# Optimization experiments

Hardware: AMD Instinct MI355X
Metric: run time of the kernel (lower is better)

Reference implementation:

```python
import jax, jax.numpy as jnp
import numpy as np

B, T, C_IN, DIM, NFFT, HOP = 8, 1024, 256, 512, 1024, 256
NOUT = NFFT // 2 + 1
BB_DIL = (1, 1, 2, 2, 4, 4, 8, 8)
RES_DIL = (1, 3, 5)
N_RES = 3


def conv1d(x, w, b, dilation=1, groups=1, padding=0):
    # x: (B,C,T), w: (O, I/groups, K)
    y = jax.lax.conv_general_dilated(
        x, w, window_strides=(1,), padding=[(padding, padding)],
        rhs_dilation=(dilation,), dimension_numbers=('NCH', 'OIH', 'NCH'),
        feature_group_count=groups)
    return y + b[None, :, None]


def layernorm(x, g, b, eps=1e-6):
    m = jnp.mean(x, -1, keepdims=True)
    v = jnp.mean((x - m) ** 2, -1, keepdims=True)
    return (x - m) * jax.lax.rsqrt(v + eps) * g + b


def istft(spec, window):
    # spec: (B, F, Tf) complex, center=True, hann window, win_length=n_fft
    Bsz, F_, Tf = spec.shape
    frames = jnp.fft.irfft(spec, n=NFFT, axis=1)            # (B, n_fft, Tf)
    frames = jnp.transpose(frames, (0, 2, 1)) * window       # (B, Tf, n_fft)
    L = NFFT + HOP * (Tf - 1)
    idx = jnp.arange(Tf)[:, None] * HOP + jnp.arange(NFFT)[None, :]  # (Tf, n_fft)
    y = jnp.zeros((Bsz, L), frames.dtype).at[:, idx].add(frames)
    env = jnp.zeros((L,), window.dtype).at[idx].add(
        jnp.broadcast_to(window ** 2, (Tf, NFFT)))
    y = y / jnp.where(env > 1e-11, env, 1.0)
    start = NFFT // 2
    return y[:, start:start + HOP * (Tf - 1)]


def setup_inputs() -> dict:
    key = jax.random.key(0)
    ks = iter(jax.random.split(key, 64))
    r = lambda *s: jax.random.normal(next(ks), s, jnp.float32) * 0.02
    return {
        'x': jax.random.normal(next(ks), (B, T, C_IN), jnp.float32),
        'conv_in_w': r(DIM, C_IN, 7), 'conv_in_b': r(DIM),
        'skip_w': r(DIM, C_IN, 1), 'skip_b': r(DIM),
        'bb_dw_w': r(8, DIM, 1, 7), 'bb_dw_b': r(8, DIM),
        'bb_ln_g': jnp.ones((8, DIM), jnp.float32), 'bb_ln_b': jnp.zeros((8, DIM), jnp.float32),
        'bb_pw1_w': r(8, 4 * DIM, DIM), 'bb_pw1_b': r(8, 4 * DIM),
        'bb_pw2_w': r(8, DIM, 4 * DIM), 'bb_pw2_b': r(8, DIM),
        'bb_gamma': jnp.full((8, DIM), 1e-6, jnp.float32),
        'res_w1': r(N_RES, 3, DIM, DIM, 3), 'res_b1': r(N_RES, 3, DIM),
        'res_w2': r(N_RES, 3, DIM, DIM, 3), 'res_b2': r(N_RES, 3, DIM),
        'ln_g': jnp.ones((DIM,), jnp.float32), 'ln_b': jnp.zeros((DIM,), jnp.float32),
        'mag_w1': r(DIM, DIM), 'mag_b1': r(DIM),
        'mag_w2': r(NOUT, DIM), 'mag_b2': r(NOUT),
        'ph_w': r(NOUT, DIM), 'ph_b': r(NOUT),
        'cumsum_w': jnp.linspace(0.05, 0.4, NOUT, dtype=jnp.float32)[None, :],
        'window': (0.5 - 0.5 * jnp.cos(2.0 * jnp.pi * jnp.arange(NFFT) / NFFT)).astype(jnp.float32),
    }


def reference(x, conv_in_w, conv_in_b, skip_w, skip_b,
              bb_dw_w, bb_dw_b, bb_ln_g, bb_ln_b,
              bb_pw1_w, bb_pw1_b, bb_pw2_w, bb_pw2_b, bb_gamma,
              res_w1, res_b1, res_w2, res_b2,
              ln_g, ln_b, mag_w1, mag_b1, mag_w2, mag_b2,
              ph_w, ph_b, cumsum_w, window):
    # (B,T,C) -> (B,C,T)
    h = jnp.transpose(x, (0, 2, 1))
    skip = conv1d(h, skip_w, skip_b)                     # (B,DIM,T)
    hp = jnp.pad(h, ((0, 0), (0, 0), (3, 3)), mode='reflect')
    h = conv1d(hp, conv_in_w, conv_in_b)                 # kernel 7, pad 0 -> (B,DIM,T)
    # ConvNeXt backbone
    for i, d in enumerate(BB_DIL):
        res = h
        pad = (7 + (d - 1) * 6) // 2
        y = conv1d(h, bb_dw_w[i], bb_dw_b[i], dilation=d, groups=DIM, padding=pad)
        y = jnp.transpose(y, (0, 2, 1))                  # (B,T,DIM)
        y = layernorm(y, bb_ln_g[i], bb_ln_b[i])
        y = jax.nn.gelu(y @ bb_pw1_w[i].T + bb_pw1_b[i], approximate=False)
        y = y @ bb_pw2_w[i].T + bb_pw2_b[i]
        y = bb_gamma[i] * y
        h = res + jnp.transpose(y, (0, 2, 1))
    h = h + skip                                         # same length T
    # Residual dilated conv stacks
    for i in range(N_RES):
        for j, d in enumerate(RES_DIL):
            y = conv1d(h, res_w1[i, j], res_b1[i, j], dilation=d, padding=d)
            y = jax.nn.leaky_relu(y, 0.1)
            y = conv1d(y, res_w2[i, j], res_b2[i, j], padding=1)
            h = h + y
    h = jnp.transpose(h, (0, 2, 1))                      # (B,T,DIM)
    h = layernorm(h, ln_g, ln_b)
    # magnitude head
    m = jax.nn.gelu(h @ mag_w1.T + mag_b1, approximate=False)
    log_mag = m @ mag_w2.T + mag_b2
    mag = jnp.exp(jnp.clip(log_mag, -10.0, 10.0))        # (B,T,NOUT)
    # instantaneous-frequency phase head
    inst = jnp.tanh(h @ ph_w.T + ph_b) * jnp.pi
    phase = jnp.cumsum(inst * cumsum_w, axis=1)
    phase = jnp.remainder(phase + jnp.pi, 2.0 * jnp.pi) - jnp.pi
    # synthesize
    spec = jax.lax.complex(mag * jnp.cos(phase), mag * jnp.sin(phase))
    spec = jnp.transpose(spec, (0, 2, 1))                # (B,F,T)
    return istft(spec, window)
```

## Files before the change

kernel.cpp:

```cpp
#include <hip/hip_runtime.h>
#include <math.h>

constexpr int Bv = 8, Tv = 1024, DIMC = 512, NOUTC = 513;
constexpr int Mrows = Bv * 1024;
constexpr int LDS_S = 1056;
constexpr float PI_F = 3.14159265358979323846f;
constexpr float TWOPI_F = 6.28318530717958647692f;

struct TapInfo { int n; int off[7]; };
struct PtrTable { _Float16* h[36]; };

enum { BND_NONE = 0, BND_ZERO, BND_REFLECT };

typedef _Float16 half8v __attribute__((ext_vector_type(8)));
typedef _Float16 half4v __attribute__((ext_vector_type(4)));
typedef float f32x4 __attribute__((ext_vector_type(4)));

__device__ __forceinline__ void gld_lds16(const void* g, void* l) {
  __builtin_amdgcn_global_load_lds(
      (const __attribute__((address_space(1))) unsigned int*)g,
      (__attribute__((address_space(3))) unsigned int*)l, 16, 0, 0);
}

__device__ __forceinline__ void xcd_tile(int TMpix, int TNpix, int& m0, int& n0) {
  const int lin = blockIdx.y * gridDim.x + blockIdx.x;
  const int cpx = (gridDim.x * gridDim.y) >> 3;
  const int nid = (lin & 7) * cpx + (lin >> 3);
  m0 = (nid / gridDim.y) * TMpix;
  n0 = (nid % gridDim.y) * TNpix;
}

enum { MEPI_GELU_H = 0, MEPI_GAMMARES };

template<int EPI, int TN>
__global__ __launch_bounds__(256)
void mfma_gemm(const _Float16* __restrict__ A, int lda,
               const _Float16* __restrict__ W, int K,
               const float* __restrict__ bias,
               const float* __restrict__ aux,
               float* __restrict__ hio,
               _Float16* __restrict__ Ch,
               int N, int ldc)
{
  constexpr int NFR = TN / 32;
  __shared__ _Float16 sA[2][128 * 32];
  __shared__ _Float16 sB[2][TN * 32];
  int m0, n0;
  xcd_tile(128, TN, m0, n0);
  const int tid = threadIdx.x;
  const int wid = tid >> 6, lane = tid & 63;
  const int wr = wid >> 1, wc = wid & 1;
  const int fr = lane & 15, fq = lane >> 4;

  f32x4 acc[4][NFR] = {};

  const int rbase = tid >> 2;
  const int kwS = (((tid & 3) ^ ((tid >> 3) & 3)) << 3);
  const int nkc = K >> 5;
  const int fqS = fq ^ ((fr >> 1) & 3);
  const int aBase = (wr * 64 + fr) * 32 + fqS * 8;
  const int bBase = (wc * (TN / 2) + fr) * 32 + fqS * 8;

  const _Float16* arow[2];
  #pragma unroll
  for (int s = 0; s < 2; ++s)
    arow[s] = A + (size_t)(m0 + s * 64 + rbase) * lda + kwS;

  auto STAGE = [&](int kc, int buf) {
    const int k0 = kc << 5;
    #pragma unroll
    for (int s = 0; s < 2; ++s)
      gld_lds16(arow[s] + k0, (char*)&sA[buf][0] + s * 4096 + wid * 1024);
    #pragma unroll
    for (int s = 0; s < TN / 64; ++s) {
      size_t bo = (size_t)(n0 + s * 64 + rbase) * K + kwS + k0;
      gld_lds16(W + bo, (char*)&sB[buf][0] + s * 4096 + wid * 1024);
    }
  };
  auto COMPUTE = [&](int buf) {
    half8v aF[4], bF[NFR];
    #pragma unroll
    for (int i = 0; i < 4; ++i) aF[i] = *(const half8v*)&sA[buf][aBase + i * 512];
    #pragma unroll
    for (int j = 0; j < NFR; ++j) bF[j] = *(const half8v*)&sB[buf][bBase + j * 512];
    #pragma unroll
    for (int i = 0; i < 4; ++i)
      #pragma unroll
      for (int j = 0; j < NFR; ++j)
        acc[i][j] = __builtin_amdgcn_mfma_f32_16x16x32_f16(aF[i], bF[j], acc[i][j], 0, 0, 0);
  };

  STAGE(0, 0);
  __syncthreads();
  int cur = 0;
  for (int kc = 0; kc < nkc; ++kc) {
    if (kc + 1 < nkc) STAGE(kc + 1, cur ^ 1);
    COMPUTE(cur);
    __syncthreads();
    cur ^= 1;
  }

  #pragma unroll
  for (int j = 0; j < NFR; ++j) {
    const int n = n0 + wc * (TN / 2) + j * 16 + fr;
    const float bj = bias[n];
    const float gj = (EPI == MEPI_GAMMARES) ? aux[n] : 0.f;
    #pragma unroll
    for (int i = 0; i < 4; ++i) {
      const int mB = m0 + wr * 64 + i * 16 + fq * 4;
      #pragma unroll
      for (int r = 0; r < 4; ++r) {
        const int m = mB + r;
        float v = acc[i][j][r] + bj;
        if (EPI == MEPI_GELU_H) {
          v = 0.5f * v * (1.f + erff(v * 0.70710678118654752f));
          Ch[(size_t)m * ldc + n] = (_Float16)v;
        } else {
          hio[(size_t)m * ldc + n] += gj * v;
        }
      }
    }
  }
}

enum { SEPI_F32 = 0, SEPI_LEAKY_SPLIT, SEPI_ADDRES_SPLIT,
       SEPI_GELU_SPLIT, SEPI_EXPCLIP, SEPI_TANHCW };

template<int EPI, int BND, int TN>
__global__ __launch_bounds__(256)
void mfma_gemm_split(const _Float16* __restrict__ Ah, const _Float16* __restrict__ Al, int lda,
                     const _Float16* __restrict__ Wh, const _Float16* __restrict__ Wl, int K,
                     const float* __restrict__ bias,
                     const float* __restrict__ aux,
                     float* __restrict__ hio,
                     float* __restrict__ Cf,
                     _Float16* __restrict__ Chh, _Float16* __restrict__ Chl,
                     int N, int ldc,
                     const _Float16* __restrict__ zpage,
                     TapInfo taps)
{
  constexpr int NFR = TN / 32;
  __shared__ _Float16 sAh[2][128 * 32];
  __shared__ _Float16 sAl[2][128 * 32];
  __shared__ _Float16 sBh[2][TN * 32];
  __shared__ _Float16 sBl[2][TN * 32];
  int m0, n0;
  xcd_tile(128, TN, m0, n0);
  const int tid = threadIdx.x;
  const int wid = tid >> 6, lane = tid & 63;
  const int wr = wid >> 1, wc = wid & 1;
  const int fr = lane & 15, fq = lane >> 4;

  f32x4 acc[4][NFR] = {};

  const int t0 = m0 & (Tv - 1);
  const int rbase = tid >> 2;
  const int kwS = (((tid & 3) ^ ((tid >> 3) & 3)) << 3);
  const int nkc = K >> 5;
  const int NT = taps.n * nkc;
  const int fqS = fq ^ ((fr >> 1) & 3);
  const int aBase = (wr * 64 + fr) * 32 + fqS * 8;
  const int bBase = (wc * (TN / 2) + fr) * 32 + fqS * 8;

  auto STAGE = [&](int st, int buf) {
    int tap = (taps.n == 1) ? 0 : (st / nkc);
    int kc = st - tap * nkc;
    const int k0 = kc << 5;
    const int off = (BND == BND_NONE) ? 0 : taps.off[tap];
    const _Float16* Wth = Wh + (size_t)tap * N * K;
    const _Float16* Wtl = Wl + (size_t)tap * N * K;
    #pragma unroll
    for (int s = 0; s < 2; ++s) {
      int t = t0 + s * 64 + rbase + off;
      bool valid = true;
      if (BND == BND_REFLECT) t = (t < 0) ? -t : (t >= Tv ? 2 * Tv - 2 - t : t);
      else if (BND == BND_ZERO) valid = (t >= 0) && (t < Tv);
      size_t ro = (size_t)(m0 - t0 + t) * lda + kwS + k0;
      const void* sh = valid ? (const void*)(Ah + ro) : (const void*)zpage;
      const void* sl = valid ? (const void*)(Al + ro) : (const void*)zpage;
      gld_lds16(sh, (char*)&sAh[buf][0] + s * 4096 + wid * 1024);
      gld_lds16(sl, (char*)&sAl[buf][0] + s * 4096 + wid * 1024);
    }
    #pragma unroll
    for (int s = 0; s < TN / 64; ++s) {
      size_t bo = (size_t)(n0 + s * 64 + rbase) * K + kwS + k0;
      gld_lds16(Wth + bo, (char*)&sBh[buf][0] + s * 4096 + wid * 1024);
      gld_lds16(Wtl + bo, (char*)&sBl[buf][0] + s * 4096 + wid * 1024);
    }
  };

  auto COMPUTE = [&](int buf) {
    half8v ah[4], al[4], bh[NFR], bl[NFR];
    #pragma unroll
    for (int i = 0; i < 4; ++i) {
      ah[i] = *(const half8v*)&sAh[buf][aBase + i * 512];
      al[i] = *(const half8v*)&sAl[buf][aBase + i * 512];
    }
    #pragma unroll
    for (int j = 0; j < NFR; ++j) {
      bh[j] = *(const half8v*)&sBh[buf][bBase + j * 512];
      bl[j] = *(const half8v*)&sBl[buf][bBase + j * 512];
    }
    #pragma unroll
    for (int i = 0; i < 4; ++i)
      #pragma unroll
      for (int j = 0; j < NFR; ++j) {
        acc[i][j] = __builtin_amdgcn_mfma_f32_16x16x32_f16(ah[i], bh[j], acc[i][j], 0, 0, 0);
        acc[i][j] = __builtin_amdgcn_mfma_f32_16x16x32_f16(ah[i], bl[j], acc[i][j], 0, 0, 0);
        acc[i][j] = __builtin_amdgcn_mfma_f32_16x16x32_f16(al[i], bh[j], acc[i][j], 0, 0, 0);
      }
  };

  STAGE(0, 0);
  __syncthreads();
  int cur = 0;
  for (int st = 0; st < NT; ++st) {
    if (st + 1 < NT) STAGE(st + 1, cur ^ 1);
    COMPUTE(cur);
    __syncthreads();
    cur ^= 1;
  }

  #pragma unroll
  for (int j = 0; j < NFR; ++j) {
    const int n = n0 + wc * (TN / 2) + j * 16 + fr;
    const bool nok = (n < N);
    const float bj = (nok && bias) ? bias[n] : 0.f;
    const float ax = (EPI == SEPI_TANHCW && nok) ? aux[n] : 0.f;
    #pragma unroll
    for (int i = 0; i < 4; ++i) {
      const int mB = m0 + wr * 64 + i * 16 + fq * 4;
      #pragma unroll
      for (int r = 0; r < 4; ++r) {
        const int m = mB + r;
        float v = acc[i][j][r] + bj;
        if (!nok) continue;
        if (EPI == SEPI_F32) {
          Cf[(size_t)m * ldc + n] = v;
        } else if (EPI == SEPI_GELU_SPLIT) {
          v = 0.5f * v * (1.f + erff(v * 0.70710678118654752f));
          _Float16 hi = (_Float16)v;
          Chh[(size_t)m * ldc + n] = hi;
          Chl[(size_t)m * ldc + n] = (_Float16)(v - (float)hi);
        } else if (EPI == SEPI_EXPCLIP) {
          Cf[(size_t)m * ldc + n] = expf(fminf(fmaxf(v, -10.f), 10.f));
        } else if (EPI == SEPI_TANHCW) {
          Cf[(size_t)m * ldc + n] = tanhf(v) * PI_F * ax;
        }
      }
    }
  }
}

enum { REPI_LEAKY = 0, REPI_ADDRES };

template<int EPI>
__global__ __launch_bounds__(256)
void res_gemm(const _Float16* __restrict__ Ah, const _Float16* __restrict__ Al,
              const _Float16* __restrict__ Wh, const _Float16* __restrict__ Wl,
              const float* __restrict__ bias,
              float* __restrict__ hio,
              _Float16* __restrict__ Chh, _Float16* __restrict__ Chl,
              const _Float16* __restrict__ zpage,
              int d)
{
  __shared__ _Float16 sAh_[160 * 32];
  __shared__ _Float16 sAl_[160 * 32];
  __shared__ _Float16 sB_[3 * 2 * 64 * 32];
  int m0, n0;
  xcd_tile(128, 64, m0, n0);
  const int tid = threadIdx.x;
  const int wid = tid >> 6, lane = tid & 63;
  const int wr = wid >> 1, wc = wid & 1;
  const int fr = lane & 15, fq = lane >> 4;
  const int t0 = m0 & (Tv - 1);

  f32x4 acc[4][2] = {};
  const int offs[3] = {-d, 0, d};

  for (int kc = 0; kc < 16; ++kc) {
    const int k0h = kc << 5;
    #pragma unroll
    for (int it = 0; it < 5; ++it) {
      int cb = it * 4 + wid;
      int half = (cb >= 10) ? 1 : 0;
      int rb = (cb - half * 10) * 16;
      int row = rb + (lane >> 2);
      int slot_g = (lane & 3) ^ ((row >> 1) & 3);
      int t = t0 - 16 + row;
      bool valid = (t >= 0) && (t < Tv);
      const _Float16* srcb = half ? Al : Ah;
      const void* src = valid
          ? (const void*)(srcb + (size_t)(m0 - t0 + t) * DIMC + k0h + slot_g * 8)
          : (const void*)(zpage + slot_g * 8);
      void* dst = (char*)(half ? sAl_ : sAh_) + rb * 64;
      gld_lds16(src, dst);
    }
    #pragma unroll
    for (int it = 0; it < 6; ++it) {
      int cb = it * 4 + wid;
      int tap = cb >> 3;
      int r2 = cb & 7;
      int half = r2 >> 2;
      int rb = (r2 & 3) * 16;
      int row = rb + (lane >> 2);
      int slot_g = (lane & 3) ^ ((row >> 1) & 3);
      const _Float16* srcb = (half ? Wl : Wh) + (size_t)tap * 512 * 512
                           + (size_t)(n0 + row) * 512 + k0h + slot_g * 8;
      void* dst = (char*)sB_ + ((size_t)(tap * 2 + half) * 64 + rb) * 64;
      gld_lds16(srcb, dst);
    }
    __syncthreads();

    #pragma unroll
    for (int tap = 0; tap < 3; ++tap) {
      const int off = offs[tap];
      half8v ah[4], al[4], bh[2], bl[2];
      #pragma unroll
      for (int i = 0; i < 4; ++i) {
        int rA = wr * 64 + i * 16 + fr + off + 16;
        int ab = rA * 64 + ((fq ^ ((rA >> 1) & 3)) * 16);
        ah[i] = *(const half8v*)((const char*)sAh_ + ab);
        al[i] = *(const half8v*)((const char*)sAl_ + ab);
      }
      #pragma unroll
      for (int j = 0; j < 2; ++j) {
        int rB = wc * 32 + j * 16 + fr;
        int bb = rB * 64 + ((fq ^ ((rB >> 1) & 3)) * 16);
        bh[j] = *(const half8v*)((const char*)sB_ + (tap * 2 + 0) * 4096 + bb);
        bl[j] = *(const half8v*)((const char*)sB_ + (tap * 2 + 1) * 4096 + bb);
      }
      #pragma unroll
      for (int i = 0; i < 4; ++i)
        #pragma unroll
        for (int j = 0; j < 2; ++j) {
          acc[i][j] = __builtin_amdgcn_mfma_f32_16x16x32_f16(ah[i], bh[j], acc[i][j], 0, 0, 0);
          acc[i][j] = __builtin_amdgcn_mfma_f32_16x16x32_f16(ah[i], bl[j], acc[i][j], 0, 0, 0);
          acc[i][j] = __builtin_amdgcn_mfma_f32_16x16x32_f16(al[i], bh[j], acc[i][j], 0, 0, 0);
        }
    }
    __syncthreads();
  }

  #pragma unroll
  for (int j = 0; j < 2; ++j) {
    const int n = n0 + wc * 32 + j * 16 + fr;
    const float bj = bias[n];
    #pragma unroll
    for (int i = 0; i < 4; ++i) {
      const int mB = m0 + wr * 64 + i * 16 + fq * 4;
      #pragma unroll
      for (int r = 0; r < 4; ++r) {
        const int m = mB + r;
        float v = acc[i][j][r] + bj;
        if (EPI == REPI_LEAKY) {
          v = (v > 0.f) ? v : 0.1f * v;
          _Float16 hi = (_Float16)v;
          Chh[(size_t)m * DIMC + n] = hi;
          Chl[(size_t)m * DIMC + n] = (_Float16)(v - (float)hi);
        } else {
          float nh = hio[(size_t)m * DIMC + n] + v;
          hio[(size_t)m * DIMC + n] = nh;
          _Float16 hi = (_Float16)nh;
          Chh[(size_t)m * DIMC + n] = hi;
          Chl[(size_t)m * DIMC + n] = (_Float16)(nh - (float)hi);
        }
      }
    }
  }
}

__global__ __launch_bounds__(256)
void convin_gemm(const _Float16* __restrict__ Ah, const _Float16* __restrict__ Al,
                 const _Float16* __restrict__ Wh, const _Float16* __restrict__ Wl,
                 const float* __restrict__ bias,
                 float* __restrict__ Cf)
{
  __shared__ _Float16 sAh_[160 * 32];
  __shared__ _Float16 sAl_[160 * 32];
  __shared__ _Float16 sB_[7 * 2 * 64 * 32];
  int m0, n0;
  xcd_tile(128, 64, m0, n0);
  const int tid = threadIdx.x;
  const int wid = tid >> 6, lane = tid & 63;
  const int wr = wid >> 1, wc = wid & 1;
  const int fr = lane & 15, fq = lane >> 4;
  const int t0 = m0 & (Tv - 1);

  f32x4 acc[4][2] = {};

  for (int kc = 0; kc < 8; ++kc) {
    const int k0h = kc << 5;
    #pragma unroll
    for (int it = 0; it < 5; ++it) {
      int cb = it * 4 + wid;
      int half = (cb >= 10) ? 1 : 0;
      int rb = (cb - half * 10) * 16;
      int row = rb + (lane >> 2);
      int slot_g = (lane & 3) ^ ((row >> 1) & 3);
      int t = t0 - 16 + row;
      t = (t < 0) ? -t : (t >= Tv ? 2 * Tv - 2 - t : t);
      const _Float16* srcb = half ? Al : Ah;
      const void* src = srcb + (size_t)(m0 - t0 + t) * 256 + k0h + slot_g * 8;
      void* dst = (char*)(half ? sAl_ : sAh_) + rb * 64;
      gld_lds16(src, dst);
    }
    #pragma unroll
    for (int it = 0; it < 14; ++it) {
      int cb = it * 4 + wid;
      int tap = cb >> 3;
      int r2 = cb & 7;
      int half = r2 >> 2;
      int rb = (r2 & 3) * 16;
      int row = rb + (lane >> 2);
      int slot_g = (lane & 3) ^ ((row >> 1) & 3);
      const _Float16* srcb = (half ? Wl : Wh) + (size_t)tap * 512 * 256
                           + (size_t)(n0 + row) * 256 + k0h + slot_g * 8;
      void* dst = (char*)sB_ + ((size_t)(tap * 2 + half) * 64 + rb) * 64;
      gld_lds16(srcb, dst);
    }
    __syncthreads();

    #pragma unroll
    for (int tap = 0; tap < 7; ++tap) {
      const int off = tap - 3;
      half8v ah[4], al[4], bh[2], bl[2];
      #pragma unroll
      for (int i = 0; i < 4; ++i) {
        int rA = wr * 64 + i * 16 + fr + off + 16;
        int ab = rA * 64 + ((fq ^ ((rA >> 1) & 3)) * 16);
        ah[i] = *(const half8v*)((const char*)sAh_ + ab);
        al[i] = *(const half8v*)((const char*)sAl_ + ab);
      }
      #pragma unroll
      for (int j = 0; j < 2; ++j) {
        int rB = wc * 32 + j * 16 + fr;
        int bb = rB * 64 + ((fq ^ ((rB >> 1) & 3)) * 16);
        bh[j] = *(const half8v*)((const char*)sB_ + (tap * 2 + 0) * 4096 + bb);
        bl[j] = *(const half8v*)((const char*)sB_ + (tap * 2 + 1) * 4096 + bb);
      }
      #pragma unroll
      for (int i = 0; i < 4; ++i)
        #pragma unroll
        for (int j = 0; j < 2; ++j) {
          acc[i][j] = __builtin_amdgcn_mfma_f32_16x16x32_f16(ah[i], bh[j], acc[i][j], 0, 0, 0);
          acc[i][j] = __builtin_amdgcn_mfma_f32_16x16x32_f16(ah[i], bl[j], acc[i][j], 0, 0, 0);
          acc[i][j] = __builtin_amdgcn_mfma_f32_16x16x32_f16(al[i], bh[j], acc[i][j], 0, 0, 0);
        }
    }
    __syncthreads();
  }

  #pragma unroll
  for (int j = 0; j < 2; ++j) {
    const int n = n0 + wc * 32 + j * 16 + fr;
    const float bj = bias[n];
    #pragma unroll
    for (int i = 0; i < 4; ++i) {
      const int mB = m0 + wr * 64 + i * 16 + fq * 4;
      #pragma unroll
      for (int r = 0; r < 4; ++r) {
        const int m = mB + r;
        Cf[(size_t)m * DIMC + n] = acc[i][j][r] + bj;
      }
    }
  }
}

__global__ __launch_bounds__(256)
void dwln(const float* __restrict__ h, const float* __restrict__ w,
          const float* __restrict__ bias, const float* __restrict__ g,
          const float* __restrict__ be, _Float16* __restrict__ out, int d)
{
  int wid = threadIdx.x >> 6, lane = threadIdx.x & 63;
  int m = (blockIdx.x << 2) + wid;
  int t = m & (Tv - 1);
  int bT = m - t;
  int c0 = lane * 8;
  float acc[8];
  {
    float4 b0 = *(const float4*)&bias[c0];
    float4 b1 = *(const float4*)&bias[c0 + 4];
    acc[0] = b0.x; acc[1] = b0.y; acc[2] = b0.z; acc[3] = b0.w;
    acc[4] = b1.x; acc[5] = b1.y; acc[6] = b1.z; acc[7] = b1.w;
  }
  #pragma unroll
  for (int k = 0; k < 7; ++k) {
    int tt = t + (k - 3) * d;
    if (tt < 0 || tt >= Tv) continue;
    const float* hp = &h[(size_t)(bT + tt) * DIMC + c0];
    float4 v0 = *(const float4*)hp;
    float4 v1 = *(const float4*)(hp + 4);
    float hv[8] = {v0.x, v0.y, v0.z, v0.w, v1.x, v1.y, v1.z, v1.w};
    #pragma unroll
    for (int q = 0; q < 8; ++q)
      acc[q] = fmaf(hv[q], w[(c0 + q) * 7 + k], acc[q]);
  }
  float sum = 0.f;
  #pragma unroll
  for (int q = 0; q < 8; ++q) sum += acc[q];
  #pragma unroll
  for (int o = 32; o > 0; o >>= 1) sum += __shfl_xor(sum, o);
  float mean = sum * (1.f / 512.f);
  float vs = 0.f;
  #pragma unroll
  for (int q = 0; q < 8; ++q) { float dd = acc[q] - mean; vs = fmaf(dd, dd, vs); }
  #pragma unroll
  for (int o = 32; o > 0; o >>= 1) vs += __shfl_xor(vs, o);
  float rstd = rsqrtf(vs * (1.f / 512.f) + 1e-6f);
  float4 g0 = *(const float4*)&g[c0];
  float4 g1 = *(const float4*)&g[c0 + 4];
  float4 e0 = *(const float4*)&be[c0];
  float4 e1 = *(const float4*)&be[c0 + 4];
  float gv[8] = {g0.x, g0.y, g0.z, g0.w, g1.x, g1.y, g1.z, g1.w};
  float ev[8] = {e0.x, e0.y, e0.z, e0.w, e1.x, e1.y, e1.z, e1.w};
  half8v ov;
  #pragma unroll
  for (int q = 0; q < 8; ++q)
    ov[q] = (_Float16)((acc[q] - mean) * rstd * gv[q] + ev[q]);
  *(half8v*)&out[(size_t)m * DIMC + c0] = ov;
}

__global__ __launch_bounds__(256)
void lnorm_split(const float* __restrict__ in, const float* __restrict__ g,
                 const float* __restrict__ be,
                 _Float16* __restrict__ ohi, _Float16* __restrict__ olo)
{
  int wid = threadIdx.x >> 6, lane = threadIdx.x & 63;
  int m = (blockIdx.x << 2) + wid;
  int c0 = lane * 8;
  const float* row = in + (size_t)m * DIMC + c0;
  float4 v0 = *(const float4*)row;
  float4 v1 = *(const float4*)(row + 4);
  float acc[8] = {v0.x, v0.y, v0.z, v0.w, v1.x, v1.y, v1.z, v1.w};
  float sum = 0.f;
  #pragma unroll
  for (int q = 0; q < 8; ++q) sum += acc[q];
  #pragma unroll
  for (int o = 32; o > 0; o >>= 1) sum += __shfl_xor(sum, o);
  float mean = sum * (1.f / 512.f);
  float vs = 0.f;
  #pragma unroll
  for (int q = 0; q < 8; ++q) { float dd = acc[q] - mean; vs = fmaf(dd, dd, vs); }
  #pragma unroll
  for (int o = 32; o > 0; o >>= 1) vs += __shfl_xor(vs, o);
  float rstd = rsqrtf(vs * (1.f / 512.f) + 1e-6f);
  float4 g0 = *(const float4*)&g[c0];
  float4 g1 = *(const float4*)&g[c0 + 4];
  float4 e0 = *(const float4*)&be[c0];
  float4 e1 = *(const float4*)&be[c0 + 4];
  float gv[8] = {g0.x, g0.y, g0.z, g0.w, g1.x, g1.y, g1.z, g1.w};
  float ev[8] = {e0.x, e0.y, e0.z, e0.w, e1.x, e1.y, e1.z, e1.w};
  half8v hv, lv;
  #pragma unroll
  for (int q = 0; q < 8; ++q) {
    float v = (acc[q] - mean) * rstd * gv[q] + ev[q];
    _Float16 hi = (_Float16)v;
    hv[q] = hi; lv[q] = (_Float16)(v - (float)hi);
  }
  *(half8v*)&ohi[(size_t)m * DIMC + c0] = hv;
  *(half8v*)&olo[(size_t)m * DIMC + c0] = lv;
}

__global__ __launch_bounds__(256)
void add_split(float* __restrict__ a, const float* __restrict__ b,
               _Float16* __restrict__ hi, _Float16* __restrict__ lo, int n)
{
  int i = (blockIdx.x * 256 + threadIdx.x) * 4;
  if (i >= n) return;
  float4 va = *(const float4*)&a[i];
  float4 vb = *(const float4*)&b[i];
  float v[4] = {va.x + vb.x, va.y + vb.y, va.z + vb.z, va.w + vb.w};
  *(float4*)&a[i] = make_float4(v[0], v[1], v[2], v[3]);
  half4v h, l;
  #pragma unroll
  for (int q = 0; q < 4; ++q) {
    _Float16 hh = (_Float16)v[q];
    h[q] = hh; l[q] = (_Float16)(v[q] - (float)hh);
  }
  *(half4v*)&hi[i] = h;
  *(half4v*)&lo[i] = l;
}

__global__ __launch_bounds__(256)
void cvt_split(const float* __restrict__ in, _Float16* __restrict__ hi,
               _Float16* __restrict__ lo, int n)
{
  int i = (blockIdx.x * 256 + threadIdx.x) * 4;
  if (i >= n) return;
  float4 vv = *(const float4*)&in[i];
  float v[4] = {vv.x, vv.y, vv.z, vv.w};
  half4v h, l;
  #pragma unroll
  for (int q = 0; q < 4; ++q) {
    _Float16 hh = (_Float16)v[q];
    h[q] = hh; l[q] = (_Float16)(v[q] - (float)hh);
  }
  *(half4v*)&hi[i] = h;
  *(half4v*)&lo[i] = l;
}

__global__ __launch_bounds__(256)
void cvt_split_pad(const float* __restrict__ in, _Float16* __restrict__ hi,
                   _Float16* __restrict__ lo, int rows, int cols, int padRows)
{
  int i = blockIdx.x * 256 + threadIdx.x;
  if (i >= padRows * cols) return;
  int r = i / cols;
  float v = (r < rows) ? in[i] : 0.f;
  _Float16 h = (_Float16)v;
  hi[i] = h; lo[i] = (_Float16)(v - (float)h);
}

__global__ __launch_bounds__(256)
void cvt_h(const float* __restrict__ in, _Float16* __restrict__ out, int n)
{
  int i = (blockIdx.x * 256 + threadIdx.x) * 4;
  if (i >= n) return;
  float4 v = *(const float4*)&in[i];
  half4v h;
  h[0] = (_Float16)v.x; h[1] = (_Float16)v.y;
  h[2] = (_Float16)v.z; h[3] = (_Float16)v.w;
  *(half4v*)&out[i] = h;
}

__global__ __launch_bounds__(256)
void repack_split(const float* __restrict__ in, _Float16* __restrict__ hi,
                  _Float16* __restrict__ lo, int O, int C, int KT)
{
  int idx = blockIdx.x * 256 + threadIdx.x;
  if (idx >= O * C) return;
  int o = idx / C, c = idx - o * C;
  for (int k = 0; k < KT; ++k) {
    float v = in[((size_t)o * C + c) * KT + k];
    _Float16 h = (_Float16)v;
    size_t dst = ((size_t)k * O + o) * C + c;
    hi[dst] = h; lo[dst] = (_Float16)(v - (float)h);
  }
}

__global__ __launch_bounds__(256)
void repack_all(const float* __restrict__ res_w1, const float* __restrict__ res_w2,
                PtrTable pt)
{
  int blk = blockIdx.x;
  int conv = blk >> 10;
  int idx = ((blk & 1023) << 8) + threadIdx.x;
  int o = idx >> 9, c = idx & 511;
  const float* src = (conv < 9) ? (res_w1 + (size_t)conv * 786432)
                                : (res_w2 + (size_t)(conv - 9) * 786432);
  _Float16* hi = pt.h[conv * 2];
  _Float16* lo = pt.h[conv * 2 + 1];
  #pragma unroll
  for (int k = 0; k < 3; ++k) {
    float v = src[((size_t)o * 512 + c) * 3 + k];
    _Float16 hh = (_Float16)v;
    size_t dst = ((size_t)k * 512 + o) * 512 + c;
    hi[dst] = hh; lo[dst] = (_Float16)(v - (float)hh);
  }
}

__global__ __launch_bounds__(256)
void zero_fill16(_Float16* __restrict__ p)
{
  int i = threadIdx.x * 8;
  #pragma unroll
  for (int q = 0; q < 8; ++q) p[i + q] = (_Float16)0.f;
}

__global__ __launch_bounds__(256)
void build_basis_split(const float* __restrict__ window,
                       _Float16* __restrict__ bhi, _Float16* __restrict__ blo)
{
  int n = blockIdx.x;
  float wn = window[n];
  const float invN = 1.f / 1024.f;
  for (int j = threadIdx.x; j < LDS_S; j += 256) {
    float coef = 0.f;
    if (j < 513) {
      int k = j;
      if (k == 0)        coef = invN;
      else if (k == 512) coef = (n & 1) ? -invN : invN;
      else {
        int r = (k * n) & 1023;
        coef = 2.f * invN * cosf(TWOPI_F * (float)r * (1.f / 1024.f));
      }
    } else if (j < 1026) {
      int k = j - 513;
      if (k != 0 && k != 512) {
        int r = (k * n) & 1023;
        coef = -2.f * invN * sinf(TWOPI_F * (float)r * (1.f / 1024.f));
      }
    }
    float v = coef * wn;
    _Float16 hi = (_Float16)v;
    bhi[(size_t)n * LDS_S + j] = hi;
    blo[(size_t)n * LDS_S + j] = (_Float16)(v - (float)hi);
  }
}

__global__ __launch_bounds__(256)
void scan_part(const float* __restrict__ dph, float* __restrict__ psum)
{
  int b = blockIdx.x, fg = blockIdx.y;
  int w = threadIdx.x >> 6, lane = threadIdx.x & 63;
  int tc = blockIdx.z * 4 + w;
  int f = fg * 64 + lane;
  if (f >= NOUTC) return;
  const float* p = dph + (size_t)(b * Tv + tc * 32) * NOUTC + f;
  float s = 0.f;
  #pragma unroll 8
  for (int j = 0; j < 32; ++j) s += p[(size_t)j * NOUTC];
  psum[((size_t)b * 32 + tc) * 520 + f] = s;
}

__global__ __launch_bounds__(256)
void scan_off(float* __restrict__ psum)
{
  int idx = blockIdx.x * 256 + threadIdx.x;
  if (idx >= 8 * NOUTC) return;
  int b = idx / NOUTC, f = idx - b * NOUTC;
  float run = 0.f;
  for (int tc = 0; tc < 32; ++tc) {
    size_t o = ((size_t)b * 32 + tc) * 520 + f;
    float v = psum[o];
    psum[o] = run;
    run += v;
  }
}

__global__ __launch_bounds__(256)
void scan_emit(const float* __restrict__ dph, const float* __restrict__ mag,
               const float* __restrict__ psum,
               _Float16* __restrict__ Shi, _Float16* __restrict__ Slo)
{
  int b = blockIdx.x, fg = blockIdx.y;
  int w = threadIdx.x >> 6, lane = threadIdx.x & 63;
  int tc = blockIdx.z * 4 + w;
  int f = fg * 64 + lane;
  if (f >= NOUTC) return;
  float run = psum[((size_t)b * 32 + tc) * 520 + f];
  const size_t base = (size_t)(b * Tv + tc * 32) * NOUTC + f;
  for (int j = 0; j < 32; ++j) {
    run += dph[base + (size_t)j * NOUTC];
    float r = fmodf(run + PI_F, TWOPI_F);
    if (r < 0.f) r += TWOPI_F;
    float wph = r - PI_F;
    float mg = mag[base + (size_t)j * NOUTC];
    float sn, cs;
    sincosf(wph, &sn, &cs);
    size_t mrow = (size_t)(b * Tv + tc * 32 + j) * LDS_S;
    float vc = mg * cs, vs2 = mg * sn;
    _Float16 hc = (_Float16)vc, hs = (_Float16)vs2;
    Shi[mrow + f] = hc;        Slo[mrow + f] = (_Float16)(vc - (float)hc);
    Shi[mrow + 513 + f] = hs;  Slo[mrow + 513 + f] = (_Float16)(vs2 - (float)hs);
  }
}

__global__ __launch_bounds__(256)
void pad_S(_Float16* __restrict__ Shi, _Float16* __restrict__ Slo)
{
  int idx = blockIdx.x * 256 + threadIdx.x;
  if (idx >= Mrows * 30) return;
  int m = idx / 30, c = 1026 + idx % 30;
  Shi[(size_t)m * LDS_S + c] = (_Float16)0.f;
  Slo[(size_t)m * LDS_S + c] = (_Float16)0.f;
}

__global__ __launch_bounds__(256)
void ola(const float* __restrict__ frames, const float* __restrict__ window,
         float* __restrict__ out)
{
  int idx = blockIdx.x * 256 + threadIdx.x;
  if (idx >= Bv * 261888) return;
  int b = idx / 261888;
  int i = idx - b * 261888;
  int l = i + 512;
  int tmax = l >> 8; if (tmax > 1023) tmax = 1023;
  int tmin = (l >= 1023) ? ((l - 1023 + 255) >> 8) : 0;
  float acc = 0.f, env = 0.f;
  for (int t = tmin; t <= tmax; ++t) {
    int n = l - (t << 8);
    acc += frames[(size_t)(b * Tv + t) * 1024 + n];
    float wv = window[n];
    env = fmaf(wv, wv, env);
  }
  out[idx] = acc / (env > 1e-11f ? env : 1.f);
}

extern "C" void kernel_launch(void* const* d_in, const int* in_sizes, int n_in,
                              void* d_out, int out_size, void* d_ws, size_t ws_size,
                              hipStream_t stream)
{
  const float* x         = (const float*)d_in[0];
  const float* conv_in_w = (const float*)d_in[1];
  const float* conv_in_b = (const float*)d_in[2];
  const float* skip_w    = (const float*)d_in[3];
  const float* skip_b    = (const float*)d_in[4];
  const float* bb_dw_w   = (const float*)d_in[5];
  const float* bb_dw_b   = (const float*)d_in[6];
  const float* bb_ln_g   = (const float*)d_in[7];
  const float* bb_ln_b   = (const float*)d_in[8];
  const float* bb_pw1_w  = (const float*)d_in[9];
  const float* bb_pw1_b  = (const float*)d_in[10];
  const float* bb_pw2_w  = (const float*)d_in[11];
  const float* bb_pw2_b  = (const float*)d_in[12];
  const float* bb_gamma  = (const float*)d_in[13];
  const float* res_w1    = (const float*)d_in[14];
  const float* res_b1    = (const float*)d_in[15];
  const float* res_w2    = (const float*)d_in[16];
  const float* res_b2    = (const float*)d_in[17];
  const float* ln_g      = (const float*)d_in[18];
  const float* ln_b      = (const float*)d_in[19];
  const float* mag_w1    = (const float*)d_in[20];
  const float* mag_b1    = (const float*)d_in[21];
  const float* mag_w2    = (const float*)d_in[22];
  const float* mag_b2    = (const float*)d_in[23];
  const float* ph_w      = (const float*)d_in[24];
  const float* ph_b      = (const float*)d_in[25];
  const float* cumsum_w  = (const float*)d_in[26];
  const float* window    = (const float*)d_in[27];
  float* out = (float*)d_out;
  float* ws  = (float*)d_ws;

  float* w_h     = ws;
  float* w_skip  = ws + 4194304;
  float* w_t4    = ws + 8388608;
  float* w_mag   = ws + 12582912;
  float* w_dph   = ws + 16785408;
  float* w_basis = ws + 20987904;
  float* w_big   = ws + 22069248;
  _Float16* t3h  = (_Float16*)w_big;
  _Float16* h_hi = (_Float16*)w_big;
  _Float16* h_lo = h_hi + 4194304;
  _Float16* y_hi = h_hi + 8388608;
  _Float16* y_lo = h_hi + 12582912;
  _Float16* Shi  = (_Float16*)w_big;
  _Float16* Slo  = Shi + 8650752;
  float* w_frames= w_h;

  _Float16* t2h  = (_Float16*)(ws + 30720000);
  _Float16* x_hi = (_Float16*)(ws + 32817152);
  _Float16* x_lo = (_Float16*)(ws + 33865728);
  _Float16* wA_hi= (_Float16*)(ws + 34914304);
  _Float16* wA_lo= (_Float16*)(ws + 35438592);
  _Float16* wB_hi= (_Float16*)(ws + 35962880);
  _Float16* wB_lo= (_Float16*)(ws + 36487168);
  _Float16* zpg  = (_Float16*)(ws + 37011456);
  float* w_psum  = ws + 37012480;

  _Float16* wpw1h = (_Float16*)w_t4;
  _Float16* wpw2h = (_Float16*)w_mag;

  static const size_t slotOffF[18] = {
    8388608, 9175040, 9961472, 10747904, 11534336,
    12582912, 13369344, 14155776, 14942208, 15728640,
    16785408, 17571840, 18358272, 19144704, 19931136,
    32817152, 33603584,
    30720000
  };
  PtrTable pt;
  for (int cv = 0; cv < 18; ++cv) {
    _Float16* hi = (_Float16*)(ws + slotOffF[cv]);
    pt.h[cv * 2] = hi;
    pt.h[cv * 2 + 1] = hi + 786432;
  }

  _Float16* lshi = (_Float16*)w_skip;
  _Float16* lslo = lshi + 4194304;
  _Float16* t4hi = (_Float16*)w_t4;
  _Float16* t4lo = t4hi + 4194304;
  _Float16* m1hi = t2h;
  _Float16* m1lo = t2h + 262144;
  _Float16* m2hi = t2h + 524288;
  _Float16* m2lo = t2h + 851968;
  _Float16* phhi = t2h + 1179648;
  _Float16* phlo = t2h + 1507328;
  _Float16* bhi  = (_Float16*)w_basis;
  _Float16* blo  = bhi + 1081344;

  dim3 blk(256);
  TapInfo tp1{1, {0}};

  zero_fill16<<<dim3(1), blk, 0, stream>>>(zpg);
  cvt_split<<<dim3(8192 * 256 / 4 / 256), blk, 0, stream>>>(x, x_hi, x_lo, 8192 * 256);
  cvt_h<<<dim3(8388608 / 4 / 256), blk, 0, stream>>>(bb_pw1_w, wpw1h, 8388608);
  cvt_h<<<dim3(8388608 / 4 / 256), blk, 0, stream>>>(bb_pw2_w, wpw2h, 8388608);

  repack_split<<<dim3(512 * 256 / 256), blk, 0, stream>>>(conv_in_w, wA_hi, wA_lo, 512, 256, 7);
  convin_gemm<<<dim3(64, 8), blk, 0, stream>>>(
      x_hi, x_lo, wA_hi, wA_lo, conv_in_b, w_h);
  repack_split<<<dim3(512 * 256 / 256), blk, 0, stream>>>(skip_w, wB_hi, wB_lo, 512, 256, 1);
  mfma_gemm_split<SEPI_F32, BND_NONE, 64><<<dim3(64, 8), blk, 0, stream>>>(
      x_hi, x_lo, 256, wB_hi, wB_lo, 256, skip_b, nullptr, nullptr, w_skip, nullptr, nullptr,
      512, 512, zpg, tp1);

  const int dil[8] = {1, 1, 2, 2, 4, 4, 8, 8};
  for (int i = 0; i < 8; ++i) {
    dwln<<<dim3(2048), blk, 0, stream>>>(w_h, bb_dw_w + i * 512 * 7, bb_dw_b + i * 512,
                                         bb_ln_g + i * 512, bb_ln_b + i * 512, t2h, dil[i]);
    mfma_gemm<MEPI_GELU_H, 128><<<dim3(64, 16), blk, 0, stream>>>(
        t2h, 512, wpw1h + (size_t)i * 2048 * 512, 512, bb_pw1_b + i * 2048,
        nullptr, nullptr, t3h, 2048, 2048);
    mfma_gemm<MEPI_GAMMARES, 64><<<dim3(64, 8), blk, 0, stream>>>(
        t3h, 2048, wpw2h + (size_t)i * 512 * 2048, 2048, bb_pw2_b + i * 512,
        bb_gamma + i * 512, w_h, nullptr, 512, 512);
  }
  add_split<<<dim3(4194304 / 4 / 256), blk, 0, stream>>>(w_h, w_skip, h_hi, h_lo, 4194304);

  repack_all<<<dim3(18 * 1024), blk, 0, stream>>>(res_w1, res_w2, pt);

  const int rdil[3] = {1, 3, 5};
  for (int i = 0; i < 3; ++i)
    for (int j = 0; j < 3; ++j) {
      int d = rdil[j];
      int idx = i * 3 + j;
      res_gemm<REPI_LEAKY><<<dim3(64, 8), blk, 0, stream>>>(
          h_hi, h_lo, pt.h[idx * 2], pt.h[idx * 2 + 1],
          res_b1 + idx * 512, nullptr, y_hi, y_lo, zpg, d);
      res_gemm<REPI_ADDRES><<<dim3(64, 8), blk, 0, stream>>>(
          y_hi, y_lo, pt.h[(9 + idx) * 2], pt.h[(9 + idx) * 2 + 1],
          res_b2 + idx * 512, w_h, h_hi, h_lo, zpg, 1);
    }

  lnorm_split<<<dim3(2048), blk, 0, stream>>>(w_h, ln_g, ln_b, lshi, lslo);

  cvt_split<<<dim3(262144 / 4 / 256), blk, 0, stream>>>(mag_w1, m1hi, m1lo, 262144);
  cvt_split_pad<<<dim3(640 * 512 / 256), blk, 0, stream>>>(mag_w2, m2hi, m2lo, 513, 512, 640);
  cvt_split_pad<<<dim3(640 * 512 / 256), blk, 0, stream>>>(ph_w, phhi, phlo, 513, 512, 640);

  mfma_gemm_split<SEPI_GELU_SPLIT, BND_NONE, 64><<<dim3(64, 8), blk, 0, stream>>>(
      lshi, lslo, 512, m1hi, m1lo, 512, mag_b1, nullptr, nullptr, nullptr,
      t4hi, t4lo, 512, 512, zpg, tp1);
  mfma_gemm_split<SEPI_EXPCLIP, BND_NONE, 64><<<dim3(64, 10), blk, 0, stream>>>(
      t4hi, t4lo, 512, m2hi, m2lo, 512, mag_b2, nullptr, nullptr, w_mag,
      nullptr, nullptr, 513, 513, zpg, tp1);
  mfma_gemm_split<SEPI_TANHCW, BND_NONE, 64><<<dim3(64, 10), blk, 0, stream>>>(
      lshi, lslo, 512, phhi, phlo, 512, ph_b, cumsum_w, nullptr, w_dph,
      nullptr, nullptr, 513, 513, zpg, tp1);

  build_basis_split<<<dim3(1024), blk, 0, stream>>>(window, bhi, blo);
  pad_S<<<dim3((Mrows * 30 + 255) / 256), blk, 0, stream>>>(Shi, Slo);
  scan_part<<<dim3(8, 9, 8), blk, 0, stream>>>(w_dph, w_psum);
  scan_off<<<dim3(17), blk, 0, stream>>>(w_psum);
  scan_emit<<<dim3(8, 9, 8), blk, 0, stream>>>(w_dph, w_mag, w_psum, Shi, Slo);
  mfma_gemm_split<SEPI_F32, BND_NONE, 128><<<dim3(64, 8), blk, 0, stream>>>(
      Shi, Slo, LDS_S, bhi, blo, LDS_S, nullptr, nullptr, nullptr, w_frames,
      nullptr, nullptr, 1024, 1024, zpg, tp1);
  ola<<<dim3((Bv * 261888 + 255) / 256), blk, 0, stream>>>(w_frames, window, out);
}
```

Before: 2.182 ms.

## Drop XCD-aware tile remap and transpose depthwise weights for vectorized loads

Removes the XCD-interleaving block-to-tile remapping in all GEMM kernels in favour of plain blockIdx-based tiles. It also adds a repack kernel that transposes the depthwise conv weights to a [layer][tap][channel] layout, so dwln can load them as float4 vectors instead of strided scalar loads. Dropping the XCD remap may hurt L2 locality on the multi-XCD MI355X, while the weight transpose adds one small launch.

```diff
diff --git a/kernel.cpp b/kernel.cpp
--- a/kernel.cpp
+++ b/kernel.cpp
@@ -20,14 +20,6 @@
   __builtin_amdgcn_global_load_lds(
       (const __attribute__((address_space(1))) unsigned int*)g,
       (__attribute__((address_space(3))) unsigned int*)l, 16, 0, 0);
-}
-
-__device__ __forceinline__ void xcd_tile(int TMpix, int TNpix, int& m0, int& n0) {
-  const int lin = blockIdx.y * gridDim.x + blockIdx.x;
-  const int cpx = (gridDim.x * gridDim.y) >> 3;
-  const int nid = (lin & 7) * cpx + (lin >> 3);
-  m0 = (nid / gridDim.y) * TMpix;
-  n0 = (nid % gridDim.y) * TNpix;
 }
 
 enum { MEPI_GELU_H = 0, MEPI_GAMMARES };
@@ -45,8 +37,8 @@
   constexpr int NFR = TN / 32;
   __shared__ _Float16 sA[2][128 * 32];
   __shared__ _Float16 sB[2][TN * 32];
-  int m0, n0;
-  xcd_tile(128, TN, m0, n0);
+  const int m0 = blockIdx.x * 128;
+  const int n0 = blockIdx.y * TN;
   const int tid = threadIdx.x;
   const int wid = tid >> 6, lane = tid & 63;
   const int wr = wid >> 1, wc = wid & 1;
@@ -144,8 +136,8 @@
   __shared__ _Float16 sAl[2][128 * 32];
   __shared__ _Float16 sBh[2][TN * 32];
   __shared__ _Float16 sBl[2][TN * 32];
-  int m0, n0;
-  xcd_tile(128, TN, m0, n0);
+  const int m0 = blockIdx.x * 128;
+  const int n0 = blockIdx.y * TN;
   const int tid = threadIdx.x;
   const int wid = tid >> 6, lane = tid & 63;
   const int wr = wid >> 1, wc = wid & 1;
@@ -267,8 +259,8 @@
   __shared__ _Float16 sAh_[160 * 32];
   __shared__ _Float16 sAl_[160 * 32];
   __shared__ _Float16 sB_[3 * 2 * 64 * 32];
-  int m0, n0;
-  xcd_tile(128, 64, m0, n0);
+  const int m0 = blockIdx.x * 128;
+  const int n0 = blockIdx.y * 64;
   const int tid = threadIdx.x;
   const int wid = tid >> 6, lane = tid & 63;
   const int wr = wid >> 1, wc = wid & 1;
@@ -379,8 +371,8 @@
   __shared__ _Float16 sAh_[160 * 32];
   __shared__ _Float16 sAl_[160 * 32];
   __shared__ _Float16 sB_[7 * 2 * 64 * 32];
-  int m0, n0;
-  xcd_tile(128, 64, m0, n0);
+  const int m0 = blockIdx.x * 128;
+  const int n0 = blockIdx.y * 64;
   const int tid = threadIdx.x;
   const int wid = tid >> 6, lane = tid & 63;
   const int wr = wid >> 1, wc = wid & 1;
@@ -468,7 +460,7 @@
 }
 
 __global__ __launch_bounds__(256)
-void dwln(const float* __restrict__ h, const float* __restrict__ w,
+void dwln(const float* __restrict__ h, const float* __restrict__ wt,
           const float* __restrict__ bias, const float* __restrict__ g,
           const float* __restrict__ be, _Float16* __restrict__ out, int d)
 {
@@ -491,10 +483,14 @@
     const float* hp = &h[(size_t)(bT + tt) * DIMC + c0];
     float4 v0 = *(const float4*)hp;
     float4 v1 = *(const float4*)(hp + 4);
+    const float* wp = &wt[k * DIMC + c0];
+    float4 w0 = *(const float4*)wp;
+    float4 w1 = *(const float4*)(wp + 4);
     float hv[8] = {v0.x, v0.y, v0.z, v0.w, v1.x, v1.y, v1.z, v1.w};
+    float wv[8] = {w0.x, w0.y, w0.z, w0.w, w1.x, w1.y, w1.z, w1.w};
     #pragma unroll
     for (int q = 0; q < 8; ++q)
-      acc[q] = fmaf(hv[q], w[(c0 + q) * 7 + k], acc[q]);
+      acc[q] = fmaf(hv[q], wv[q], acc[q]);
   }
   float sum = 0.f;
   #pragma unroll
@@ -519,6 +515,17 @@
   for (int q = 0; q < 8; ++q)
     ov[q] = (_Float16)((acc[q] - mean) * rstd * gv[q] + ev[q]);
   *(half8v*)&out[(size_t)m * DIMC + c0] = ov;
+}
+
+__global__ __launch_bounds__(256)
+void repack_dw(const float* __restrict__ in, float* __restrict__ out)
+{
+  int idx = blockIdx.x * 256 + threadIdx.x;
+  if (idx >= 8 * 512 * 7) return;
+  int l = idx / 3584;
+  int r = idx - l * 3584;
+  int c = r / 7, k = r - c * 7;
+  out[l * 3584 + k * 512 + c] = in[idx];
 }
 
 __global__ __launch_bounds__(256)
@@ -848,6 +855,7 @@
   _Float16* wB_lo= (_Float16*)(ws + 36487168);
   _Float16* zpg  = (_Float16*)(ws + 37011456);
   float* w_psum  = ws + 37012480;
+  float* w_dwT   = ws + 37145600;
 
   _Float16* wpw1h = (_Float16*)w_t4;
   _Float16* wpw2h = (_Float16*)w_mag;
@@ -886,6 +894,7 @@
   cvt_split<<<dim3(8192 * 256 / 4 / 256), blk, 0, stream>>>(x, x_hi, x_lo, 8192 * 256);
   cvt_h<<<dim3(8388608 / 4 / 256), blk, 0, stream>>>(bb_pw1_w, wpw1h, 8388608);
   cvt_h<<<dim3(8388608 / 4 / 256), blk, 0, stream>>>(bb_pw2_w, wpw2h, 8388608);
+  repack_dw<<<dim3(112), blk, 0, stream>>>(bb_dw_w, w_dwT);
 
   repack_split<<<dim3(512 * 256 / 256), blk, 0, stream>>>(conv_in_w, wA_hi, wA_lo, 512, 256, 7);
   convin_gemm<<<dim3(64, 8), blk, 0, stream>>>(
@@ -897,7 +906,7 @@
 
   const int dil[8] = {1, 1, 2, 2, 4, 4, 8, 8};
   for (int i = 0; i < 8; ++i) {
-    dwln<<<dim3(2048), blk, 0, stream>>>(w_h, bb_dw_w + i * 512 * 7, bb_dw_b + i * 512,
+    dwln<<<dim3(2048), blk, 0, stream>>>(w_h, w_dwT + i * 3584, bb_dw_b + i * 512,
                                          bb_ln_g + i * 512, bb_ln_b + i * 512, t2h, dil[i]);
     mfma_gemm<MEPI_GELU_H, 128><<<dim3(64, 16), blk, 0, stream>>>(
         t2h, 512, wpw1h + (size_t)i * 2048 * 512, 512, bb_pw1_b + i * 2048,
```

New measurement: 1.865 ms. 1.17x faster.
